# Kernel tuning notes

Measured on AMD Instinct MI355X. Metric: run time of the kernel, lower is better.

## Reference

```python
import jax, jax.numpy as jnp
import numpy as np

B, S, D = 2, 2048, 2048
H, G = 16, 4
HD = D // H          # head_dim = 128
KV = HD * G          # 512


def setup_inputs() -> dict:
    key = jax.random.key(0)
    ks = jax.random.split(key, 5)
    scale = 1.0 / np.sqrt(D)
    return {
        "x": jax.random.normal(ks[0], (B, S, D), dtype=jnp.float32),
        "Wqkv": jax.random.normal(ks[1], (D, D + 2 * KV), dtype=jnp.float32) * scale,
        "bqkv": jax.random.normal(ks[2], (D + 2 * KV,), dtype=jnp.float32) * 0.01,
        "Wout": jax.random.normal(ks[3], (D, D), dtype=jnp.float32) * scale,
        "bout": jax.random.normal(ks[4], (D,), dtype=jnp.float32) * 0.01,
    }


def reference(x, Wqkv, bqkv, Wout, bout):
    b, s, _ = x.shape
    qkv = x @ Wqkv + bqkv                                  # [b, s, D + 2*KV]
    q, k, v = jnp.split(qkv, [D, D + KV], axis=-1)
    q = q.reshape(b, s, H, HD)                             # [b, s, H, hd]
    # torch .repeat tiles the group axis: head h -> group (h % G)
    k = jnp.tile(k.reshape(b, s, G, HD), (1, 1, H // G, 1))  # [b, s, H, hd]
    v = jnp.tile(v.reshape(b, s, G, HD), (1, 1, H // G, 1))
    # NOTE: original divides by head_dim (not sqrt(head_dim)) -- kept faithfully
    scores = jnp.einsum("bqhd,bkhd->bhqk", q, k) / HD      # [b, H, s, s]
    prob = jax.nn.softmax(scores, axis=-1)
    out = jnp.einsum("bhqk,bkhd->bqhd", prob, v).reshape(b, s, D)
    return out @ Wout + bout
```

## Files before the change

kernel.cpp:

```cpp
#include <hip/hip_runtime.h>
#include <stdint.h>

typedef __bf16 bf16;
typedef __bf16 bf16x8 __attribute__((ext_vector_type(8)));
typedef __bf16 bf16x4 __attribute__((ext_vector_type(4)));
typedef __bf16 bf16x2 __attribute__((ext_vector_type(2)));
typedef float  f32x4  __attribute__((ext_vector_type(4)));

#define B_   2
#define S_   2048
#define D_   2048
#define H_   16
#define G_   4
#define HD_  128
#define KV_  512
#define NQKV 3072
#define M_   4096

__device__ __forceinline__ void async16(bf16* lds, const bf16* g) {
  __builtin_amdgcn_global_load_lds(
      (const __attribute__((address_space(1))) unsigned int*)g,
      (__attribute__((address_space(3))) unsigned int*)lds, 16, 0, 0);
}

__device__ __forceinline__ f32x4 mfma16(bf16x8 a, bf16x8 b, f32x4 c) {
  return __builtin_amdgcn_mfma_f32_16x16x32_bf16(a, b, c, 0, 0, 0);
}

__global__ __launch_bounds__(256) void prep_kernel(const float* __restrict__ x,
                                                   const float* __restrict__ Wqkv,
                                                   const float* __restrict__ Wout,
                                                   bf16* __restrict__ xb,
                                                   bf16* __restrict__ wqkvT,
                                                   bf16* __restrict__ woutT) {
  __shared__ float ldst[32][65];
  int bid = blockIdx.x;
  int t = threadIdx.x;

  if (bid < 8192) {
    int i = bid * 256 + t;
    float4 v = ((const float4*)x)[i];
    bf16x4 o = { (bf16)v.x, (bf16)v.y, (bf16)v.z, (bf16)v.w };
    *(bf16x4*)(xb + (size_t)i * 4) = o;
    return;
  }
  bid -= 8192;

  const float* src; bf16* dst; int rows, cols, nct;
  if (bid < 3072) { src = Wqkv; dst = wqkvT; rows = 2048; cols = 3072; nct = 96; }
  else { bid -= 3072; src = Wout; dst = woutT; rows = 2048; cols = 2048; nct = 64; }

  int bc = (bid % nct) * 32;
  int br = (bid / nct) * 64;
  int c = t & 31, rb = t >> 5;
  #pragma unroll
  for (int i = 0; i < 8; i++)
    ldst[c][i * 8 + rb] = src[(size_t)(br + i * 8 + rb) * cols + bc + c];
  __syncthreads();
  #pragma unroll
  for (int i = 0; i < 4; i++) {
    int oc = i * 8 + rb;
    bf16x2 v2 = { (bf16)ldst[oc][2 * c], (bf16)ldst[oc][2 * c + 1] };
    *(bf16x2*)&dst[(size_t)(bc + oc) * rows + br + 2 * c] = v2;
  }
}

__global__ void transpose_v_kernel(const bf16* __restrict__ qkv,
                                   bf16* __restrict__ vt) {
  __shared__ bf16 tile[32][33];
  int bg = blockIdx.z; int b = bg / G_, g = bg % G_;
  int sb = blockIdx.x * 32, db = blockIdx.y * 32;
  int tx = threadIdx.x, ty = threadIdx.y;
  const bf16* src = qkv + (size_t)b * S_ * NQKV + (D_ + KV_ + g * HD_);
  #pragma unroll
  for (int i = 0; i < 32; i += 8)
    tile[ty + i][tx] = src[(size_t)(sb + ty + i) * NQKV + db + tx];
  __syncthreads();
  bf16* dst = vt + (size_t)(b * G_ + g) * HD_ * S_;
  int txp = ((tx & 15) >> 2) * 8 + (tx >> 4) * 4 + (tx & 3);
  #pragma unroll
  for (int i = 0; i < 32; i += 8)
    dst[(size_t)(db + ty + i) * S_ + sb + txp] = tile[tx][ty + i];
}

template <int OUT_BF16>
__global__ __launch_bounds__(256) void gemm_bt(const bf16* __restrict__ A,
                                               const bf16* __restrict__ Bt,
                                               const float* __restrict__ bias,
                                               void* __restrict__ Cout,
                                               int Ndim, int K) {
  __shared__ __align__(16) bf16 As[128 * 32];
  __shared__ __align__(16) bf16 Bs[128 * 32];
  int t = threadIdx.x;
  int w = t >> 6, l = t & 63, lr = l & 15, lg = l >> 4;
  int wm = w >> 1, wn = w & 1;
  int row0 = blockIdx.x * 128, col0 = blockIdx.y * 128;

  f32x4 acc[4][4] = {};

  const bf16* ga = A  + (size_t)(row0 + (t >> 2)) * K + (t & 3) * 8;
  const bf16* gb = Bt + (size_t)(col0 + (t >> 2)) * K + (t & 3) * 8;

  for (int k0 = 0; k0 < K; k0 += 32) {
    __syncthreads();
    #pragma unroll
    for (int i = 0; i < 2; i++)
      async16(&As[w * 512 + i * 2048], ga + (size_t)i * 64 * K + k0);
    #pragma unroll
    for (int i = 0; i < 2; i++)
      async16(&Bs[w * 512 + i * 2048], gb + (size_t)i * 64 * K + k0);
    __syncthreads();

    bf16x8 af[4], bfr[4];
    #pragma unroll
    for (int mi = 0; mi < 4; mi++)
      af[mi] = *(const bf16x8*)&As[(wm * 64 + mi * 16 + lr) * 32 + lg * 8];
    #pragma unroll
    for (int ni = 0; ni < 4; ni++)
      bfr[ni] = *(const bf16x8*)&Bs[(wn * 64 + ni * 16 + lr) * 32 + lg * 8];
    #pragma unroll
    for (int mi = 0; mi < 4; mi++)
      #pragma unroll
      for (int ni = 0; ni < 4; ni++)
        acc[mi][ni] = mfma16(af[mi], bfr[ni], acc[mi][ni]);
  }

  float bv[4];
  #pragma unroll
  for (int ni = 0; ni < 4; ni++)
    bv[ni] = bias[col0 + wn * 64 + ni * 16 + lr];

  #pragma unroll
  for (int mi = 0; mi < 4; mi++)
    #pragma unroll
    for (int ni = 0; ni < 4; ni++)
      #pragma unroll
      for (int r = 0; r < 4; r++) {
        int row = row0 + wm * 64 + mi * 16 + lg * 4 + r;
        int col = col0 + wn * 64 + ni * 16 + lr;
        float v = acc[mi][ni][r] + bv[ni];
        if (OUT_BF16)
          ((bf16*)Cout)[(size_t)row * Ndim + col] = (bf16)v;
        else
          ((float*)Cout)[(size_t)row * Ndim + col] = v;
      }
}

__global__ __launch_bounds__(256, 2) void attn_kernel(const bf16* __restrict__ qkv,
                                                      const bf16* __restrict__ vt,
                                                      bf16* __restrict__ attnb) {
  __shared__ __align__(16) bf16 Ks[2][64 * 128];
  __shared__ __align__(16) bf16 Vs[3][128 * 64];

  int t = threadIdx.x, w = t >> 6, l = t & 63, lr = l & 15, lg = l >> 4;
  int rsw = lr & 7;
  int lin = blockIdx.x + gridDim.x * blockIdx.y;
  int swz = (lin & 7) * 64 + (lin >> 3);
  int q0 = (swz & 15) * 128;
  int hb2 = swz >> 4;
  int b = hb2 >> 4, gh = hb2 & 15;
  int g = gh >> 2, h = (gh & 3) * 4 + g;

  bf16x8 qf[2][4];
  #pragma unroll
  for (int mi = 0; mi < 2; mi++) {
    const bf16* qbase = qkv + (size_t)(b * S_ + q0 + w * 32 + mi * 16 + lr) * NQKV + h * HD_;
    #pragma unroll
    for (int kc = 0; kc < 4; kc++)
      qf[mi][kc] = *(const bf16x8*)(qbase + kc * 32 + lg * 8);
  }

  const bf16* kbase = qkv + (size_t)b * S_ * NQKV + D_ + g * HD_;
  const bf16* vbase = vt + (size_t)(b * G_ + g) * HD_ * S_;

  int krowi = w * 4 + (l >> 4);
  int ksw = (l & 15) ^ (krowi & 7);
  const bf16* kgl = kbase + (size_t)krowi * NQKV + ksw * 8;
  int vrowi = w * 8 + (l >> 3);
  int vsw = (l & 7) ^ ((l >> 3) & 7);
  const bf16* vgl = vbase + (size_t)vrowi * S_ + vsw * 8;

  auto STAGE_K = [&](int nb, int kv0) {
    #pragma unroll
    for (int i = 0; i < 4; i++)
      async16(&Ks[nb][w * 512 + i * 2048], kgl + (size_t)(kv0 + i * 16) * NQKV);
  };
  auto STAGE_V = [&](bf16* vb, int kv0) {
    #pragma unroll
    for (int i = 0; i < 4; i++)
      async16(&vb[w * 512 + i * 2048], vgl + (size_t)(i * 32) * S_ + kv0);
  };

  f32x4 accO[2][8] = {};
  f32x4 accL[2] = {};
  bf16x8 paA[2][2], paB[2][2];
  bf16x8 vone;
  #pragma unroll
  for (int j = 0; j < 8; j++) vone[j] = (bf16)1.0f;

#define QKT_BLOCK(KSBUF, PAC)                                                \
  {                                                                          \
    const bf16* ks = (KSBUF);                                                \
    __builtin_amdgcn_s_setprio(1);                                           \
    _Pragma("unroll")                                                        \
    for (int fk = 0; fk < 4; fk++) {                                         \
      bf16x8 kf[4];                                                          \
      _Pragma("unroll")                                                      \
      for (int kc = 0; kc < 4; kc++)                                         \
        kf[kc] = *(const bf16x8*)&ks[(fk * 16 + lr) * 128 +                  \
                                     (((kc * 4 + lg) ^ rsw) * 8)];           \
      f32x4 sacc[2] = {};                                                    \
      _Pragma("unroll")                                                      \
      for (int mi = 0; mi < 2; mi++)                                         \
        _Pragma("unroll")                                                    \
        for (int kc = 0; kc < 4; kc++)                                       \
          sacc[mi] = mfma16(kf[kc], qf[mi][kc], sacc[mi]);                   \
      _Pragma("unroll")                                                      \
      for (int mi = 0; mi < 2; mi++) {                                       \
        float p0 = __expf(sacc[mi][0] * 0.0078125f);                         \
        float p1 = __expf(sacc[mi][1] * 0.0078125f);                         \
        float p2 = __expf(sacc[mi][2] * 0.0078125f);                         \
        float p3 = __expf(sacc[mi][3] * 0.0078125f);                         \
        PAC[mi][fk >> 1][(fk & 1) * 4 + 0] = (bf16)p0;                       \
        PAC[mi][fk >> 1][(fk & 1) * 4 + 1] = (bf16)p1;                       \
        PAC[mi][fk >> 1][(fk & 1) * 4 + 2] = (bf16)p2;                       \
        PAC[mi][fk >> 1][(fk & 1) * 4 + 3] = (bf16)p3;                       \
      }                                                                      \
    }                                                                        \
    __builtin_amdgcn_s_setprio(0);                                           \
  }

#define PV_BLOCK(PAP, VSBUF)                                                 \
  {                                                                          \
    const bf16* vsp = (VSBUF);                                               \
    __builtin_amdgcn_s_setprio(1);                                           \
    _Pragma("unroll")                                                        \
    for (int fd = 0; fd < 8; fd++) {                                         \
      bf16x8 vfr[2];                                                         \
      _Pragma("unroll")                                                      \
      for (int kk = 0; kk < 2; kk++)                                         \
        vfr[kk] = *(const bf16x8*)&vsp[(fd * 16 + lr) * 64 +                 \
                                       (((kk * 4 + lg) ^ rsw) * 8)];         \
      _Pragma("unroll")                                                      \
      for (int mi = 0; mi < 2; mi++)                                         \
        _Pragma("unroll")                                                    \
        for (int kk = 0; kk < 2; kk++)                                       \
          accO[mi][fd] = mfma16(PAP[mi][kk], vfr[kk], accO[mi][fd]);         \
    }                                                                        \
    _Pragma("unroll")                                                        \
    for (int mi = 0; mi < 2; mi++)                                           \
      _Pragma("unroll")                                                      \
      for (int kk = 0; kk < 2; kk++)                                         \
        accL[mi] = mfma16(PAP[mi][kk], vone, accL[mi]);                      \
    __builtin_amdgcn_s_setprio(0);                                           \
  }

#define BODY(TI, PAP, PAC, VPREV, VNEXT)                                     \
  {                                                                          \
    __syncthreads();                                                         \
    if ((TI) + 1 < S_ / 64) {                                                \
      STAGE_K(((TI) + 1) & 1, ((TI) + 1) * 64);                              \
      STAGE_V((VNEXT), ((TI) + 1) * 64);                                     \
    }                                                                        \
    PV_BLOCK(PAP, VPREV);                                                    \
    QKT_BLOCK(&Ks[(TI) & 1][0], PAC);                                        \
  }

  STAGE_K(0, 0);
  STAGE_V(&Vs[0][0], 0);
  __syncthreads();
  STAGE_K(1, 64);
  STAGE_V(&Vs[1][0], 64);
  QKT_BLOCK(&Ks[0][0], paA);

  bf16* vp = &Vs[0][0];
  bf16* vc = &Vs[1][0];
  bf16* vn = &Vs[2][0];

  for (int ti = 1; ti < 31; ti += 2) {
    BODY(ti,     paA, paB, vp, vn);
    BODY(ti + 1, paB, paA, vc, vp);
    bf16* tmp = vp; vp = vn; vn = vc; vc = tmp;
  }
  BODY(31, paA, paB, vp, vn);
  PV_BLOCK(paB, vc);

#undef QKT_BLOCK
#undef PV_BLOCK
#undef BODY

  #pragma unroll
  for (int mi = 0; mi < 2; mi++) {
    float rls[4];
    #pragma unroll
    for (int r = 0; r < 4; r++) rls[r] = 1.f / accL[mi][r];
    bf16* obase = attnb + (size_t)(b * S_ + q0 + w * 32 + mi * 16) * D_ + h * HD_;
    #pragma unroll
    for (int r = 0; r < 4; r++)
      #pragma unroll
      for (int fd = 0; fd < 8; fd++)
        obase[(size_t)(lg * 4 + r) * D_ + fd * 16 + lr] =
            (bf16)(accO[mi][fd][r] * rls[r]);
  }
}

extern "C" void kernel_launch(void* const* d_in, const int* in_sizes, int n_in,
                              void* d_out, int out_size, void* d_ws, size_t ws_size,
                              hipStream_t stream) {
  const float* x    = (const float*)d_in[0];
  const float* Wqkv = (const float*)d_in[1];
  const float* bqkv = (const float*)d_in[2];
  const float* Wout = (const float*)d_in[3];
  const float* bout = (const float*)d_in[4];
  float* out = (float*)d_out;

  char* p = (char*)d_ws;
  bf16* xb    = (bf16*)p; p += (size_t)M_ * D_ * 2;
  bf16* wqkvT = (bf16*)p; p += (size_t)NQKV * D_ * 2;
  bf16* woutT = (bf16*)p; p += (size_t)D_ * D_ * 2;
  bf16* qkvb  = (bf16*)p; p += (size_t)M_ * NQKV * 2;
  bf16* vtb   = (bf16*)p; p += (size_t)B_ * G_ * HD_ * S_ * 2;
  bf16* attnb = (bf16*)p; p += (size_t)M_ * D_ * 2;

  prep_kernel<<<dim3(13312), dim3(256), 0, stream>>>(
      x, Wqkv, Wout, xb, wqkvT, woutT);

  gemm_bt<1><<<dim3(M_ / 128, NQKV / 128), dim3(256), 0, stream>>>(xb, wqkvT, bqkv, (void*)qkvb, NQKV, D_);

  transpose_v_kernel<<<dim3(S_ / 32, HD_ / 32, B_ * G_), dim3(32, 8), 0, stream>>>(qkvb, vtb);

  attn_kernel<<<dim3(S_ / 128, B_ * H_), dim3(256), 0, stream>>>(qkvb, vtb, attnb);

  gemm_bt<0><<<dim3(M_ / 128, D_ / 128), dim3(256), 0, stream>>>(attnb, woutT, bout, (void*)out, D_, D_);
}
```

Measured before the change: 208.1 us.

## Add 256x256-tile double-buffered GEMM with split-K halves for QKV projection

```diff
diff --git a/kernel.cpp b/kernel.cpp
--- a/kernel.cpp
+++ b/kernel.cpp
@@ -81,6 +81,119 @@
   #pragma unroll
   for (int i = 0; i < 32; i += 8)
     dst[(size_t)(db + ty + i) * S_ + sb + txp] = tile[tx][ty + i];
+}
+
+template <int OUT_BF16>
+__global__ __launch_bounds__(512, 2) void gemm_kh(const bf16* __restrict__ A,
+                                                  const bf16* __restrict__ Bt,
+                                                  const float* __restrict__ bias,
+                                                  void* __restrict__ Cout,
+                                                  int Ndim, int K, int nbm) {
+  __shared__ __align__(16) bf16 As[2][2][256 * 32];
+  __shared__ __align__(16) bf16 Bs[2][2][256 * 32];
+
+  int t = threadIdx.x, w = t >> 6, l = t & 63, lr = l & 15, lg = l >> 4;
+  int wm = w >> 1, wn = w & 1;
+
+  int cpx = (int)gridDim.x >> 3;
+  int swz = ((int)blockIdx.x & 7) * cpx + ((int)blockIdx.x >> 3);
+  int row0 = (swz % nbm) * 256, col0 = (swz / nbm) * 256;
+
+  int r = w * 16 + (l >> 2);
+  int csw = (l & 3) ^ (r & 3);
+  const bf16* gA = A  + (size_t)(row0 + r) * K + csw * 8;
+  const bf16* gB = Bt + (size_t)(col0 + r) * K + csw * 8;
+
+  auto stageA = [&](int nb, int kt, int kh) {
+    const bf16* s = gA + (size_t)kt * 64 + kh * 32;
+    async16(&As[nb][kh][w * 512], s);
+    async16(&As[nb][kh][w * 512 + 4096], s + (size_t)128 * K);
+  };
+  auto stageB = [&](int nb, int kt, int kh) {
+    const bf16* s = gB + (size_t)kt * 64 + kh * 32;
+    async16(&Bs[nb][kh][w * 512], s);
+    async16(&Bs[nb][kh][w * 512 + 4096], s + (size_t)128 * K);
+  };
+
+#define LDA(mi, kc) (*(const bf16x8*)&As[c][(kc)][(wm * 64 + (mi) * 16 + lr) * 32 + ((lg ^ (lr & 3)) * 8)])
+#define LDB(ni, kc) (*(const bf16x8*)&Bs[c][(kc)][(wn * 128 + (ni) * 16 + lr) * 32 + ((lg ^ (lr & 3)) * 8)])
+
+  const int NT = K >> 6;
+  f32x4 acc[4][8] = {};
+
+  stageA(0, 0, 0); stageB(0, 0, 0); stageA(0, 0, 1); stageB(0, 0, 1);
+
+  for (int kt = 0; kt < NT; ++kt) {
+    int c = kt & 1, n = c ^ 1;
+    bool st = (kt + 1) < NT;
+
+    asm volatile("s_waitcnt vmcnt(4)" ::: "memory");
+    __builtin_amdgcn_sched_barrier(0);
+    __builtin_amdgcn_s_barrier();
+    __builtin_amdgcn_sched_barrier(0);
+
+    if (st) { stageA(n, kt + 1, 0); stageB(n, kt + 1, 0); }
+
+    {
+      bf16x8 af[4], bfr[8];
+      #pragma unroll
+      for (int mi = 0; mi < 4; mi++) af[mi] = LDA(mi, 0);
+      #pragma unroll
+      for (int ni = 0; ni < 8; ni++) bfr[ni] = LDB(ni, 0);
+      __builtin_amdgcn_s_setprio(1);
+      #pragma unroll
+      for (int mi = 0; mi < 4; mi++)
+        #pragma unroll
+        for (int ni = 0; ni < 8; ni++)
+          acc[mi][ni] = mfma16(af[mi], bfr[ni], acc[mi][ni]);
+      __builtin_amdgcn_s_setprio(0);
+    }
+
+    if (st) { asm volatile("s_waitcnt vmcnt(4)" ::: "memory"); }
+    else    { asm volatile("s_waitcnt vmcnt(0)" ::: "memory"); }
+    __builtin_amdgcn_sched_barrier(0);
+    __builtin_amdgcn_s_barrier();
+    __builtin_amdgcn_sched_barrier(0);
+
+    if (st) { stageA(n, kt + 1, 1); stageB(n, kt + 1, 1); }
+
+    {
+      bf16x8 af[4], bfr[8];
+      #pragma unroll
+      for (int mi = 0; mi < 4; mi++) af[mi] = LDA(mi, 1);
+      #pragma unroll
+      for (int ni = 0; ni < 8; ni++) bfr[ni] = LDB(ni, 1);
+      __builtin_amdgcn_s_setprio(1);
+      #pragma unroll
+      for (int mi = 0; mi < 4; mi++)
+        #pragma unroll
+        for (int ni = 0; ni < 8; ni++)
+          acc[mi][ni] = mfma16(af[mi], bfr[ni], acc[mi][ni]);
+      __builtin_amdgcn_s_setprio(0);
+    }
+  }
+#undef LDA
+#undef LDB
+
+  float bv[8];
+  #pragma unroll
+  for (int ni = 0; ni < 8; ni++)
+    bv[ni] = bias[col0 + wn * 128 + ni * 16 + lr];
+
+  #pragma unroll
+  for (int mi = 0; mi < 4; mi++)
+    #pragma unroll
+    for (int ni = 0; ni < 8; ni++)
+      #pragma unroll
+      for (int rr = 0; rr < 4; rr++) {
+        int row = row0 + wm * 64 + mi * 16 + lg * 4 + rr;
+        int col = col0 + wn * 128 + ni * 16 + lr;
+        float v = acc[mi][ni][rr] + bv[ni];
+        if (OUT_BF16)
+          ((bf16*)Cout)[(size_t)row * Ndim + col] = (bf16)v;
+        else
+          ((float*)Cout)[(size_t)row * Ndim + col] = v;
+      }
 }
 
 template <int OUT_BF16>
@@ -325,7 +438,8 @@
   prep_kernel<<<dim3(13312), dim3(256), 0, stream>>>(
       x, Wqkv, Wout, xb, wqkvT, woutT);
 
-  gemm_bt<1><<<dim3(M_ / 128, NQKV / 128), dim3(256), 0, stream>>>(xb, wqkvT, bqkv, (void*)qkvb, NQKV, D_);
+  gemm_kh<1><<<dim3((M_ / 256) * (NQKV / 256)), dim3(512), 0, stream>>>(
+      xb, wqkvT, bqkv, (void*)qkvb, NQKV, D_, M_ / 256);
 
   transpose_v_kernel<<<dim3(S_ / 32, HD_ / 32, B_ * G_), dim3(32, 8), 0, stream>>>(qkvb, vtb);
 
```

Measured after the change: 224.0 us. 7.7% more time.
